# Performance work log

Hardware: AMD Instinct MI355X
Metric: run time of the kernel (lower is better)

Reference implementation:

```python
import jax, jax.numpy as jnp
import numpy as np

DIM = 768
NUM_HEADS = 8
ETA = 1e-5
LN_EPS = 1e-5
NORM_EPS = 1e-12  # torch F.normalize clamp_min


def setup_inputs() -> dict:
    key = jax.random.key(0)
    ks = jax.random.split(key, 4)
    B, N, C = 8, 4096, DIM
    x = jax.random.normal(ks[0], (B, N, C), dtype=jnp.float32)
    # torch nn.Linear weight layout: [out, in]; qkv_bias=False per init_kwargs
    qkv_w = jax.random.normal(ks[1], (3 * C, C), dtype=jnp.float32) * (C ** -0.5)
    proj_w = jax.random.normal(ks[2], (C, C), dtype=jnp.float32) * (C ** -0.5)
    proj_b = jnp.zeros((C,), dtype=jnp.float32)
    ln_g = jnp.ones((C,), dtype=jnp.float32)
    ln_b = jnp.zeros((C,), dtype=jnp.float32)
    temperature = jnp.ones((NUM_HEADS, 1, 1), dtype=jnp.float32)
    gamma1 = jnp.full((C,), ETA, dtype=jnp.float32)
    return {"x": x, "qkv_w": qkv_w, "proj_w": proj_w, "proj_b": proj_b,
            "ln_g": ln_g, "ln_b": ln_b, "temperature": temperature, "gamma1": gamma1}


def _l2norm(t):
    # torch F.normalize(dim=-1): t / max(||t||_2, eps)
    n = jnp.sqrt(jnp.sum(t * t, axis=-1, keepdims=True))
    return t / jnp.maximum(n, NORM_EPS)


def reference(x, qkv_w, proj_w, proj_b, ln_g, ln_b, temperature, gamma1):
    B, N, C = x.shape
    H = NUM_HEADS
    dh = C // H
    m = x
    # LayerNorm
    mu = jnp.mean(x, axis=-1, keepdims=True)
    var = jnp.mean(jnp.square(x - mu), axis=-1, keepdims=True)
    xn = (x - mu) * jax.lax.rsqrt(var + LN_EPS) * ln_g + ln_b
    # qkv: [B,N,3C] -> [3,B,H,dh,N] (q/k/v already transposed to channels-first)
    qkv = jnp.einsum('bnc,oc->bno', xn, qkv_w)
    qkv = qkv.reshape(B, N, 3, H, dh).transpose(2, 0, 3, 4, 1)  # [3,B,H,dh,N]
    q, k, v = qkv[0], qkv[1], qkv[2]
    q = _l2norm(q)  # normalize over tokens (last dim = N)
    k = _l2norm(k)
    # cross-covariance attention over channels: [B,H,dh,dh]
    attn = jnp.einsum('bhdn,bhen->bhde', q, k) * temperature
    attn = jax.nn.softmax(attn, axis=-1)
    # weighted channel mix: [B,H,dh,N] -> [B,N,C]
    out = jnp.einsum('bhde,bhen->bhdn', attn, v)
    out = out.transpose(0, 3, 1, 2).reshape(B, N, C)
    out = jnp.einsum('bnc,oc->bno', out, proj_w) + proj_b
    out = gamma1 * out
    return out + m
```

## Files before the change

kernel.cpp:

```cpp
#include <hip/hip_runtime.h>
#include <hip/hip_bf16.h>
#include <stdint.h>

typedef __attribute__((ext_vector_type(8))) short short8;
typedef __attribute__((ext_vector_type(4))) float f32x4;
typedef __attribute__((ext_vector_type(4))) unsigned short us4;

#define DIMC 768
#define NTOK 32768
#define NPB 4096
#define HEADS 8
#define DH 96

__device__ __forceinline__ ushort f2bf(float f) {
    union { float f; uint32_t u; } c; c.f = f;
    uint32_t u = c.u;
    u += 0x7fffu + ((u >> 16) & 1u);
    return (ushort)(u >> 16);
}
__device__ __forceinline__ float bf2f(ushort h) {
    union { uint32_t u; float f; } c; c.u = ((uint32_t)h) << 16;
    return c.f;
}

__device__ __forceinline__ void gload_lds16(const void* g, void* l) {
    __builtin_amdgcn_global_load_lds(
        (const __attribute__((address_space(1))) void*)g,
        (__attribute__((address_space(3))) void*)l, 16, 0, 0);
}

__device__ __forceinline__ void gemm256_core(
    const char* aglob, const char* bglob, char* lds, f32x4 (&acc)[8][4]) {
    const int tid = threadIdx.x;
    const int lane = tid & 63, wid = tid >> 6;
    const int wr = wid >> 2, wc = wid & 3;
    const int k8 = lane >> 4, l15 = lane & 15;

    const int L0 = tid * 16, L1 = (512 + tid) * 16;
    const int S0 = L0 ^ (((L0 >> 9) & 1) << 5);
    const int S1 = L1 ^ (((L1 >> 9) & 1) << 5);
    const int sr0 = S0 >> 6, sc0 = S0 & 63;
    const int sr1 = S1 >> 6, sc1 = S1 & 63;

    int aoff[8], boff[4];
#pragma unroll
    for (int m = 0; m < 8; m++) {
        int row = wr * 128 + m * 16 + l15;
        int o = row * 64 + k8 * 16;
        aoff[m] = o ^ (((o >> 9) & 1) << 5);
    }
#pragma unroll
    for (int n = 0; n < 4; n++) {
        int row = wc * 64 + n * 16 + l15;
        int o = row * 64 + k8 * 16;
        boff[n] = o ^ (((o >> 9) & 1) << 5);
    }

#define STG_A(kt, c) do {                                     \
        const char* ak_ = aglob + (size_t)(kt) * 64;          \
        char* al_ = lds + (c) * 16384;                        \
        gload_lds16(ak_ + sr0 * 1536 + sc0, al_ + L0);        \
        gload_lds16(ak_ + sr1 * 1536 + sc1, al_ + L1);        \
    } while (0)
#define STG_B(kt, c) do {                                     \
        const char* bk_ = bglob + (size_t)(kt) * 64;          \
        char* bl_ = lds + 32768 + (c) * 16384;                \
        gload_lds16(bk_ + sr0 * 1536 + sc0, bl_ + L0);        \
        gload_lds16(bk_ + sr1 * 1536 + sc1, bl_ + L1);        \
    } while (0)
#define MFMA16(mb)                                                                 \
    __builtin_amdgcn_s_setprio(1);                                                 \
    _Pragma("unroll")                                                              \
    for (int m_ = 0; m_ < 4; m_++)                                                 \
        _Pragma("unroll")                                                          \
        for (int n_ = 0; n_ < 4; n_++)                                             \
            acc[(mb) + m_][n_] = __builtin_amdgcn_mfma_f32_16x16x32_bf16(          \
                af[m_], bf[n_], acc[(mb) + m_][n_], 0, 0, 0);                      \
    __builtin_amdgcn_s_setprio(0);
#define BAR  asm volatile("s_barrier" ::: "memory")
#define LGKM0 do { asm volatile("s_waitcnt lgkmcnt(0)" ::: "memory"); \
                   __builtin_amdgcn_sched_barrier(0); } while (0)

    STG_B(0, 0); STG_A(0, 0); STG_B(1, 1);
    asm volatile("s_waitcnt vmcnt(2)" ::: "memory");
    BAR;

    const char* a0 = lds;
    const char* a1 = lds + 16384;
    const char* b0 = lds + 32768;
    const char* b1 = lds + 49152;

#pragma unroll
    for (int i = 0; i < 6; ++i) {
        short8 af[4], bf[4];
#pragma unroll
        for (int n = 0; n < 4; n++) bf[n] = *(const short8*)(b0 + boff[n]);
#pragma unroll
        for (int m = 0; m < 4; m++) af[m] = *(const short8*)(a0 + aoff[m]);
        STG_A(2 * i + 1, 1);
        BAR;
        LGKM0;
        MFMA16(0)
        BAR;
#pragma unroll
        for (int m = 0; m < 4; m++) af[m] = *(const short8*)(a0 + aoff[4 + m]);
        if (2 * i + 2 < 12) STG_B(2 * i + 2, 0);
        BAR;
        LGKM0;
        MFMA16(4)
        if (i < 5) asm volatile("s_waitcnt vmcnt(2)" ::: "memory");
        else       asm volatile("s_waitcnt vmcnt(0)" ::: "memory");
        BAR;
#pragma unroll
        for (int n = 0; n < 4; n++) bf[n] = *(const short8*)(b1 + boff[n]);
#pragma unroll
        for (int m = 0; m < 4; m++) af[m] = *(const short8*)(a1 + aoff[m]);
        if (2 * i + 2 < 12) STG_A(2 * i + 2, 0);
        BAR;
        LGKM0;
        MFMA16(0)
        BAR;
#pragma unroll
        for (int m = 0; m < 4; m++) af[m] = *(const short8*)(a1 + aoff[4 + m]);
        if (2 * i + 3 < 12) STG_B(2 * i + 3, 1);
        BAR;
        LGKM0;
        MFMA16(4)
        if (i < 5) {
            asm volatile("s_waitcnt vmcnt(2)" ::: "memory");
            BAR;
        }
    }
#undef STG_A
#undef STG_B
#undef MFMA16
#undef BAR
#undef LGKM0
}

__global__ __launch_bounds__(256) void prep_fused_kernel(
    const float* __restrict__ qw, const float* __restrict__ pw,
    ushort* __restrict__ qwb, ushort* __restrict__ pwb,
    const float* __restrict__ x, const float* __restrict__ g,
    const float* __restrict__ b, ushort* __restrict__ xb) {
    int bid = blockIdx.x;
    if (bid < 1728) {
        int i4 = (bid * 256 + threadIdx.x) * 4;
        if (i4 < 3 * DIMC * DIMC) {
            float4 w = *(const float4*)&qw[i4];
            us4 o;
            o[0] = f2bf(w.x); o[1] = f2bf(w.y); o[2] = f2bf(w.z); o[3] = f2bf(w.w);
            *(us4*)&qwb[i4] = o;
        }
        if (i4 < DIMC * DIMC) {
            float4 w = *(const float4*)&pw[i4];
            us4 o;
            o[0] = f2bf(w.x); o[1] = f2bf(w.y); o[2] = f2bf(w.z); o[3] = f2bf(w.w);
            *(us4*)&pwb[i4] = o;
        }
        return;
    }
    int t = (bid - 1728) * 4 + (threadIdx.x >> 6);
    int lane = threadIdx.x & 63;
    const float* xr = x + (size_t)t * DIMC;
    float4 v[3];
    float s = 0.f, s2 = 0.f;
#pragma unroll
    for (int u = 0; u < 3; u++) {
        v[u] = *(const float4*)&xr[u * 256 + lane * 4];
        s  += v[u].x + v[u].y + v[u].z + v[u].w;
        s2 += v[u].x * v[u].x + v[u].y * v[u].y + v[u].z * v[u].z + v[u].w * v[u].w;
    }
#pragma unroll
    for (int off = 32; off > 0; off >>= 1) {
        s  += __shfl_down(s, off);
        s2 += __shfl_down(s2, off);
    }
    s = __shfl(s, 0);
    s2 = __shfl(s2, 0);
    float mean = s * (1.0f / DIMC);
    float rstd = rsqrtf(s2 * (1.0f / DIMC) - mean * mean + 1e-5f);
    ushort* xo = xb + (size_t)t * DIMC;
#pragma unroll
    for (int u = 0; u < 3; u++) {
        float4 gv = *(const float4*)&g[u * 256 + lane * 4];
        float4 bv = *(const float4*)&b[u * 256 + lane * 4];
        us4 o;
        o[0] = f2bf((v[u].x - mean) * rstd * gv.x + bv.x);
        o[1] = f2bf((v[u].y - mean) * rstd * gv.y + bv.y);
        o[2] = f2bf((v[u].z - mean) * rstd * gv.z + bv.z);
        o[3] = f2bf((v[u].w - mean) * rstd * gv.w + bv.w);
        *(us4*)&xo[u * 256 + lane * 4] = o;
    }
}

__global__ __launch_bounds__(512) void gemm_qkv_kernel(
    const ushort* __restrict__ xb, const ushort* __restrict__ wb,
    ushort* __restrict__ qb, ushort* __restrict__ kb, ushort* __restrict__ vb) {
    __shared__ __align__(16) char lds[65536];
    int orig = blockIdx.x;
    int wg = (orig & 7) * 144 + (orig >> 3);
    int nt = wg % 9, mt = wg / 9;
    int m0 = mt * 256, n0 = nt * 256;
    f32x4 acc[8][4] = {};
    gemm256_core((const char*)(xb + (size_t)m0 * DIMC),
                 (const char*)(wb + (size_t)n0 * DIMC), lds, acc);

    int tid = threadIdx.x, lane = tid & 63, wid = tid >> 6;
    int wr = wid >> 2, wc = wid & 3;
    int k8 = lane >> 4, l15 = lane & 15;
    int seg = n0 / DIMC;
#pragma unroll
    for (int m8 = 0; m8 < 8; m8++) {
        int r0 = m0 + wr * 128 + m8 * 16 + k8 * 4;
        int b_ = r0 >> 12, nn = r0 & (NPB - 1);
#pragma unroll
        for (int n = 0; n < 4; n++) {
            int o = n0 + wc * 64 + n * 16 + l15;
            f32x4 a = acc[m8][n];
            if (seg == 2) {
                int oL = o - 2 * DIMC;
#pragma unroll
                for (int qq = 0; qq < 4; qq++)
                    vb[(size_t)(r0 + qq) * DIMC + oL] = f2bf(a[qq]);
            } else {
                int oL = o - seg * DIMC;
                int h = oL / DH, d = oL - h * DH;
                us4 pk;
#pragma unroll
                for (int qq = 0; qq < 4; qq++) pk[qq] = f2bf(a[qq]);
                *(us4*)((seg ? kb : qb) +
                        ((size_t)(b_ * HEADS + h) * DH + d) * NPB + nn) = pk;
            }
        }
    }
}

__global__ __launch_bounds__(576) void attn_qk_kernel(
    const ushort* __restrict__ qb, const ushort* __restrict__ kb,
    float* __restrict__ S, float* __restrict__ S2) {
    int bh = blockIdx.x, ch = blockIdx.y;
    int tid = threadIdx.x, wid = tid >> 6, lane = tid & 63;
    int wr = wid / 3, wc = wid - wr * 3;
    int k8 = lane >> 4, l15 = lane & 15;
    const ushort* qrow = qb + (size_t)bh * DH * NPB + ch * 512;
    const ushort* krow = kb + (size_t)bh * DH * NPB + ch * 512;
    bool doq = (wc == 0), dok = (wr == 0);
    f32x4 acc[2][2] = {};
    float sq[2] = {0.f, 0.f}, sk[2] = {0.f, 0.f};
    for (int n = 0; n < 512; n += 32) {
        short8 a[2], b[2];
#pragma unroll
        for (int i = 0; i < 2; i++)
            a[i] = *(const short8*)&qrow[(size_t)(wr * 32 + i * 16 + l15) * NPB + n + k8 * 8];
#pragma unroll
        for (int j = 0; j < 2; j++)
            b[j] = *(const short8*)&krow[(size_t)(wc * 32 + j * 16 + l15) * NPB + n + k8 * 8];
        if (doq) {
#pragma unroll
            for (int i = 0; i < 2; i++)
#pragma unroll
                for (int u = 0; u < 8; u++) {
                    float f = bf2f((ushort)a[i][u]); sq[i] += f * f;
                }
        }
        if (dok) {
#pragma unroll
            for (int j = 0; j < 2; j++)
#pragma unroll
                for (int u = 0; u < 8; u++) {
                    float f = bf2f((ushort)b[j][u]); sk[j] += f * f;
                }
        }
#pragma unroll
        for (int i = 0; i < 2; i++)
#pragma unroll
            for (int j = 0; j < 2; j++)
                acc[i][j] = __builtin_amdgcn_mfma_f32_16x16x32_bf16(a[i], b[j], acc[i][j], 0, 0, 0);
    }
    float* S2o = S2 + ((size_t)ch * 64 + bh) * 192;
    if (doq) {
#pragma unroll
        for (int i = 0; i < 2; i++) {
            float v = sq[i];
            v += __shfl_xor(v, 16); v += __shfl_xor(v, 32);
            if (lane < 16) S2o[wr * 32 + i * 16 + l15] = v;
        }
    }
    if (dok) {
#pragma unroll
        for (int j = 0; j < 2; j++) {
            float v = sk[j];
            v += __shfl_xor(v, 16); v += __shfl_xor(v, 32);
            if (lane < 16) S2o[96 + wc * 32 + j * 16 + l15] = v;
        }
    }
    float* So = S + ((size_t)ch * 64 + bh) * (DH * DH);
#pragma unroll
    for (int i = 0; i < 2; i++)
#pragma unroll
        for (int j = 0; j < 2; j++) {
            int e = wc * 32 + j * 16 + l15;
#pragma unroll
            for (int qq = 0; qq < 4; qq++) {
                int d = wr * 32 + i * 16 + k8 * 4 + qq;
                So[d * DH + e] = acc[i][j][qq];
            }
        }
}

__global__ __launch_bounds__(192) void attn_soft_kernel(
    const float* __restrict__ S, const float* __restrict__ S2,
    const float* __restrict__ temp, ushort* __restrict__ attnT) {
    int bh = blockIdx.x, ds0 = blockIdx.y * 32;
    int tid = threadIdx.x, r = tid & 31, p = tid >> 5;
    int d = ds0 + r;
    __shared__ float rkv[96];
    if (tid < 96) {
        float sum = 0.f;
#pragma unroll 1
        for (int ch = 0; ch < 8; ch++)
            sum += S2[((size_t)ch * 64 + bh) * 192 + 96 + tid];
        rkv[tid] = 1.0f / fmaxf(sqrtf(sum), 1e-12f);
    }
    float sqd = 0.f;
#pragma unroll 1
    for (int ch = 0; ch < 8; ch++)
        sqd += S2[((size_t)ch * 64 + bh) * 192 + d];
    float rqd = 1.0f / fmaxf(sqrtf(sqd), 1e-12f);
    float4 v[4] = {};
#pragma unroll 1
    for (int ch = 0; ch < 8; ch++) {
        const float* So = S + (((size_t)ch * 64 + bh) * DH + d) * DH + p * 16;
#pragma unroll
        for (int u = 0; u < 4; u++) {
            float4 w = *(const float4*)&So[u * 4];
            v[u].x += w.x; v[u].y += w.y; v[u].z += w.z; v[u].w += w.w;
        }
    }
    __syncthreads();
    float sd = rqd * temp[bh & (HEADS - 1)];
#pragma unroll
    for (int u = 0; u < 4; u++) {
        int e0 = p * 16 + u * 4;
        v[u].x *= sd * rkv[e0]; v[u].y *= sd * rkv[e0 + 1];
        v[u].z *= sd * rkv[e0 + 2]; v[u].w *= sd * rkv[e0 + 3];
    }
    __shared__ float red[32][8], red2[32][8];
    float lm = -3.4e38f;
#pragma unroll
    for (int u = 0; u < 4; u++)
        lm = fmaxf(lm, fmaxf(fmaxf(v[u].x, v[u].y), fmaxf(v[u].z, v[u].w)));
    red[r][p] = lm;
    __syncthreads();
    float m = red[r][0];
#pragma unroll
    for (int u = 1; u < 6; u++) m = fmaxf(m, red[r][u]);
    float s = 0.f;
#pragma unroll
    for (int u = 0; u < 4; u++) {
        v[u].x = __expf(v[u].x - m); v[u].y = __expf(v[u].y - m);
        v[u].z = __expf(v[u].z - m); v[u].w = __expf(v[u].w - m);
        s += v[u].x + v[u].y + v[u].z + v[u].w;
    }
    red2[r][p] = s;
    __syncthreads();
    float tot = red2[r][0];
#pragma unroll
    for (int u = 1; u < 6; u++) tot += red2[r][u];
    float inv = 1.0f / tot;
    ushort* ao = attnT + (size_t)bh * (DH * DH) + d;
#pragma unroll
    for (int u = 0; u < 4; u++) {
        int e0 = p * 16 + u * 4;
        ao[(e0 + 0) * DH] = f2bf(v[u].x * inv);
        ao[(e0 + 1) * DH] = f2bf(v[u].y * inv);
        ao[(e0 + 2) * DH] = f2bf(v[u].z * inv);
        ao[(e0 + 3) * DH] = f2bf(v[u].w * inv);
    }
}

__global__ __launch_bounds__(256) void w2prep_kernel(
    const ushort* __restrict__ pwb, const ushort* __restrict__ attnT,
    ushort* __restrict__ W2) {
    int bh = blockIdx.x, o0 = blockIdx.y * 256;
    int b_ = bh >> 3, h = bh & 7;
    int tid = threadIdx.x, wid = tid >> 6, lane = tid & 63;
    int k8 = lane >> 4, l15 = lane & 15;
    const ushort* at = attnT + (size_t)bh * (DH * DH);
    f32x4 acc[4][6] = {};
#pragma unroll
    for (int kk = 0; kk < DH; kk += 32) {
        short8 af[4], bf[6];
#pragma unroll
        for (int m = 0; m < 4; m++)
            af[m] = *(const short8*)&pwb[(size_t)(o0 + wid * 64 + m * 16 + l15) * DIMC
                                         + h * DH + kk + k8 * 8];
#pragma unroll
        for (int n = 0; n < 6; n++)
            bf[n] = *(const short8*)&at[(n * 16 + l15) * DH + kk + k8 * 8];
#pragma unroll
        for (int m = 0; m < 4; m++)
#pragma unroll
            for (int n = 0; n < 6; n++)
                acc[m][n] = __builtin_amdgcn_mfma_f32_16x16x32_bf16(af[m], bf[n], acc[m][n], 0, 0, 0);
    }
    ushort* wo = W2 + (size_t)b_ * DIMC * DIMC + (size_t)h * DH;
#pragma unroll
    for (int m = 0; m < 4; m++) {
        int orow = o0 + wid * 64 + m * 16 + k8 * 4;
#pragma unroll
        for (int n = 0; n < 6; n++) {
            int e = n * 16 + l15;
#pragma unroll
            for (int qq = 0; qq < 4; qq++)
                wo[(size_t)(orow + qq) * DIMC + e] = f2bf(acc[m][n][qq]);
        }
    }
}

__global__ __launch_bounds__(512) void vproj_kernel(
    const ushort* __restrict__ vb, const ushort* __restrict__ W2,
    const float* __restrict__ pb, const float* __restrict__ g1,
    const float* __restrict__ x, float* __restrict__ out) {
    __shared__ __align__(16) char lds[65536];
    int orig = blockIdx.x;
    int wg = (orig & 7) * 48 + (orig >> 3);
    int b_ = wg / 48, rem = wg % 48, mt = rem / 3, ntl = rem % 3;
    int tok0 = b_ * NPB + mt * 256, o0 = ntl * 256;
    f32x4 acc[8][4] = {};
    gemm256_core((const char*)(vb + (size_t)tok0 * DIMC),
                 (const char*)(W2 + (size_t)b_ * DIMC * DIMC + (size_t)o0 * DIMC),
                 lds, acc);

    int tid = threadIdx.x, lane = tid & 63, wid = tid >> 6;
    int wr = wid >> 2, wc = wid & 3;
    int k8 = lane >> 4, l15 = lane & 15;
#pragma unroll
    for (int m8 = 0; m8 < 8; m8++) {
        int r0 = tok0 + wr * 128 + m8 * 16 + k8 * 4;
#pragma unroll
        for (int n = 0; n < 4; n++) {
            int o = o0 + wc * 64 + n * 16 + l15;
            float pbo = pb[o], g1o = g1[o];
            f32x4 a = acc[m8][n];
#pragma unroll
            for (int qq = 0; qq < 4; qq++) {
                size_t idx = (size_t)(r0 + qq) * DIMC + o;
                out[idx] = g1o * (a[qq] + pbo) + x[idx];
            }
        }
    }
}

extern "C" void kernel_launch(void* const* d_in, const int* in_sizes, int n_in,
                              void* d_out, int out_size, void* d_ws, size_t ws_size,
                              hipStream_t stream) {
    const float* x     = (const float*)d_in[0];
    const float* qkvw  = (const float*)d_in[1];
    const float* projw = (const float*)d_in[2];
    const float* projb = (const float*)d_in[3];
    const float* lng   = (const float*)d_in[4];
    const float* lnb   = (const float*)d_in[5];
    const float* temp  = (const float*)d_in[6];
    const float* g1    = (const float*)d_in[7];
    float* out = (float*)d_out;

    char* w = (char*)d_ws;
    ushort* qb    = (ushort*)(w + 0);
    ushort* kb    = (ushort*)(w + 50331648);
    ushort* vb    = (ushort*)(w + 100663296);
    ushort* qwb   = (ushort*)(w + 150994944);
    ushort* pwb   = (ushort*)(w + 154533888);
    float*  S2    = (float*)(w + 155713536);
    ushort* attnT = qwb;
    ushort* W2    = qb;
    ushort* xb    = (ushort*)d_out;
    float*  S     = (float*)((char*)d_out + 50331648);

    hipLaunchKernelGGL(prep_fused_kernel, dim3(9920), dim3(256), 0, stream,
                       qkvw, projw, qwb, pwb, x, lng, lnb, xb);
    hipLaunchKernelGGL(gemm_qkv_kernel, dim3(1152), dim3(512), 0, stream,
                       xb, qwb, qb, kb, vb);
    hipLaunchKernelGGL(attn_qk_kernel, dim3(64, 8), dim3(576), 0, stream,
                       qb, kb, S, S2);
    hipLaunchKernelGGL(attn_soft_kernel, dim3(64, 3), dim3(192), 0, stream,
                       S, S2, temp, attnT);
    hipLaunchKernelGGL(w2prep_kernel, dim3(64, 3), dim3(256), 0, stream,
                       pwb, attnT, W2);
    hipLaunchKernelGGL(vproj_kernel, dim3(384), dim3(512), 0, stream,
                       vb, W2, projb, g1, x, out);
}
```

Baseline: 253.5 us.

## Fuse softmax and W2 prep into one kernel, store partial scores as bf16

The separate softmax and W2-prep kernels are merged into one attn_finish kernel with one block per batch-head. The softmaxed attention now stays in LDS and feeds the MFMA projection directly, which drops a launch and a global round trip. The partial QK score tiles are also written as bf16 instead of fp32, halving that traffic. In exchange the fused stage runs only 64 blocks instead of 192 per stage, so parallelism is lower, and summing bf16 partials across chunks costs some precision.

```diff
diff --git a/kernel.cpp b/kernel.cpp
--- a/kernel.cpp
+++ b/kernel.cpp
@@ -238,7 +238,7 @@
 
 __global__ __launch_bounds__(576) void attn_qk_kernel(
     const ushort* __restrict__ qb, const ushort* __restrict__ kb,
-    float* __restrict__ S, float* __restrict__ S2) {
+    ushort* __restrict__ S, float* __restrict__ S2) {
     int bh = blockIdx.x, ch = blockIdx.y;
     int tid = threadIdx.x, wid = tid >> 6, lane = tid & 63;
     int wr = wid / 3, wc = wid - wr * 3;
@@ -295,7 +295,7 @@
             if (lane < 16) S2o[96 + wc * 32 + j * 16 + l15] = v;
         }
     }
-    float* So = S + ((size_t)ch * 64 + bh) * (DH * DH);
+    ushort* So = S + ((size_t)ch * 64 + bh) * (DH * DH);
 #pragma unroll
     for (int i = 0; i < 2; i++)
 #pragma unroll
@@ -304,18 +304,22 @@
 #pragma unroll
             for (int qq = 0; qq < 4; qq++) {
                 int d = wr * 32 + i * 16 + k8 * 4 + qq;
-                So[d * DH + e] = acc[i][j][qq];
+                So[d * DH + e] = f2bf(acc[i][j][qq]);
             }
         }
 }
 
-__global__ __launch_bounds__(192) void attn_soft_kernel(
-    const float* __restrict__ S, const float* __restrict__ S2,
-    const float* __restrict__ temp, ushort* __restrict__ attnT) {
-    int bh = blockIdx.x, ds0 = blockIdx.y * 32;
-    int tid = threadIdx.x, r = tid & 31, p = tid >> 5;
-    int d = ds0 + r;
+__global__ __launch_bounds__(576) void attn_finish_kernel(
+    const ushort* __restrict__ S, const float* __restrict__ S2,
+    const float* __restrict__ temp, const ushort* __restrict__ pwb,
+    ushort* __restrict__ W2) {
+    int bh = blockIdx.x;
+    int b_ = bh >> 3, h = bh & 7;
+    int tid = threadIdx.x;
     __shared__ float rkv[96];
+    __shared__ float red[96][6], red2[96][6];
+    __shared__ ushort atl[96][104];
+    int r = tid % 96, p = tid / 96;
     if (tid < 96) {
         float sum = 0.f;
 #pragma unroll 1
@@ -326,31 +330,29 @@
     float sqd = 0.f;
 #pragma unroll 1
     for (int ch = 0; ch < 8; ch++)
-        sqd += S2[((size_t)ch * 64 + bh) * 192 + d];
+        sqd += S2[((size_t)ch * 64 + bh) * 192 + r];
     float rqd = 1.0f / fmaxf(sqrtf(sqd), 1e-12f);
-    float4 v[4] = {};
+    float v[16];
+#pragma unroll
+    for (int u = 0; u < 16; u++) v[u] = 0.f;
 #pragma unroll 1
     for (int ch = 0; ch < 8; ch++) {
-        const float* So = S + (((size_t)ch * 64 + bh) * DH + d) * DH + p * 16;
-#pragma unroll
-        for (int u = 0; u < 4; u++) {
-            float4 w = *(const float4*)&So[u * 4];
-            v[u].x += w.x; v[u].y += w.y; v[u].z += w.z; v[u].w += w.w;
+        const ushort* So = S + ((size_t)ch * 64 + bh) * (DH * DH) + r * DH + p * 16;
+        short8 w0 = *(const short8*)So;
+        short8 w1 = *(const short8*)(So + 8);
+#pragma unroll
+        for (int u = 0; u < 8; u++) {
+            v[u] += bf2f((ushort)w0[u]);
+            v[8 + u] += bf2f((ushort)w1[u]);
         }
     }
     __syncthreads();
-    float sd = rqd * temp[bh & (HEADS - 1)];
-#pragma unroll
-    for (int u = 0; u < 4; u++) {
-        int e0 = p * 16 + u * 4;
-        v[u].x *= sd * rkv[e0]; v[u].y *= sd * rkv[e0 + 1];
-        v[u].z *= sd * rkv[e0 + 2]; v[u].w *= sd * rkv[e0 + 3];
-    }
-    __shared__ float red[32][8], red2[32][8];
-    float lm = -3.4e38f;
-#pragma unroll
-    for (int u = 0; u < 4; u++)
-        lm = fmaxf(lm, fmaxf(fmaxf(v[u].x, v[u].y), fmaxf(v[u].z, v[u].w)));
+    float sd = rqd * temp[h];
+#pragma unroll
+    for (int u = 0; u < 16; u++) v[u] *= sd * rkv[p * 16 + u];
+    float lm = v[0];
+#pragma unroll
+    for (int u = 1; u < 16; u++) lm = fmaxf(lm, v[u]);
     red[r][p] = lm;
     __syncthreads();
     float m = red[r][0];
@@ -358,63 +360,53 @@
     for (int u = 1; u < 6; u++) m = fmaxf(m, red[r][u]);
     float s = 0.f;
 #pragma unroll
-    for (int u = 0; u < 4; u++) {
-        v[u].x = __expf(v[u].x - m); v[u].y = __expf(v[u].y - m);
-        v[u].z = __expf(v[u].z - m); v[u].w = __expf(v[u].w - m);
-        s += v[u].x + v[u].y + v[u].z + v[u].w;
-    }
+    for (int u = 0; u < 16; u++) { v[u] = __expf(v[u] - m); s += v[u]; }
     red2[r][p] = s;
     __syncthreads();
     float tot = red2[r][0];
 #pragma unroll
     for (int u = 1; u < 6; u++) tot += red2[r][u];
     float inv = 1.0f / tot;
-    ushort* ao = attnT + (size_t)bh * (DH * DH) + d;
-#pragma unroll
-    for (int u = 0; u < 4; u++) {
-        int e0 = p * 16 + u * 4;
-        ao[(e0 + 0) * DH] = f2bf(v[u].x * inv);
-        ao[(e0 + 1) * DH] = f2bf(v[u].y * inv);
-        ao[(e0 + 2) * DH] = f2bf(v[u].z * inv);
-        ao[(e0 + 3) * DH] = f2bf(v[u].w * inv);
-    }
-}
-
-__global__ __launch_bounds__(256) void w2prep_kernel(
-    const ushort* __restrict__ pwb, const ushort* __restrict__ attnT,
-    ushort* __restrict__ W2) {
-    int bh = blockIdx.x, o0 = blockIdx.y * 256;
-    int b_ = bh >> 3, h = bh & 7;
-    int tid = threadIdx.x, wid = tid >> 6, lane = tid & 63;
-    int k8 = lane >> 4, l15 = lane & 15;
-    const ushort* at = attnT + (size_t)bh * (DH * DH);
-    f32x4 acc[4][6] = {};
-#pragma unroll
-    for (int kk = 0; kk < DH; kk += 32) {
-        short8 af[4], bf[6];
-#pragma unroll
-        for (int m = 0; m < 4; m++)
-            af[m] = *(const short8*)&pwb[(size_t)(o0 + wid * 64 + m * 16 + l15) * DIMC
-                                         + h * DH + kk + k8 * 8];
-#pragma unroll
-        for (int n = 0; n < 6; n++)
-            bf[n] = *(const short8*)&at[(n * 16 + l15) * DH + kk + k8 * 8];
-#pragma unroll
-        for (int m = 0; m < 4; m++)
-#pragma unroll
-            for (int n = 0; n < 6; n++)
-                acc[m][n] = __builtin_amdgcn_mfma_f32_16x16x32_bf16(af[m], bf[n], acc[m][n], 0, 0, 0);
-    }
-    ushort* wo = W2 + (size_t)b_ * DIMC * DIMC + (size_t)h * DH;
-#pragma unroll
-    for (int m = 0; m < 4; m++) {
-        int orow = o0 + wid * 64 + m * 16 + k8 * 4;
-#pragma unroll
-        for (int n = 0; n < 6; n++) {
-            int e = n * 16 + l15;
-#pragma unroll
-            for (int qq = 0; qq < 4; qq++)
-                wo[(size_t)(orow + qq) * DIMC + e] = f2bf(acc[m][n][qq]);
+#pragma unroll
+    for (int u = 0; u < 16; u++)
+        atl[p * 16 + u][r] = f2bf(v[u] * inv);
+    __syncthreads();
+    int wid = tid >> 6, lane = tid & 63;
+    if (wid < 8) {
+        int k8 = lane >> 4, l15 = lane & 15;
+        ushort* wo = W2 + (size_t)b_ * DIMC * DIMC + (size_t)h * DH;
+#pragma unroll
+        for (int pass = 0; pass < 2; pass++) {
+            int o0 = wid * 96 + pass * 48;
+            f32x4 acc[3][6] = {};
+#pragma unroll
+            for (int kk = 0; kk < DH; kk += 32) {
+                short8 af[3], bf[6];
+#pragma unroll
+                for (int mm = 0; mm < 3; mm++)
+                    af[mm] = *(const short8*)&pwb[(size_t)(o0 + mm * 16 + l15) * DIMC
+                                                  + h * DH + kk + k8 * 8];
+#pragma unroll
+                for (int n = 0; n < 6; n++)
+                    bf[n] = *(const short8*)&atl[n * 16 + l15][kk + k8 * 8];
+#pragma unroll
+                for (int mm = 0; mm < 3; mm++)
+#pragma unroll
+                    for (int n = 0; n < 6; n++)
+                        acc[mm][n] = __builtin_amdgcn_mfma_f32_16x16x32_bf16(
+                            af[mm], bf[n], acc[mm][n], 0, 0, 0);
+            }
+#pragma unroll
+            for (int mm = 0; mm < 3; mm++) {
+                int orow = o0 + mm * 16 + k8 * 4;
+#pragma unroll
+                for (int n = 0; n < 6; n++) {
+                    int e = n * 16 + l15;
+#pragma unroll
+                    for (int qq = 0; qq < 4; qq++)
+                        wo[(size_t)(orow + qq) * DIMC + e] = f2bf(acc[mm][n][qq]);
+                }
+            }
         }
     }
 }
@@ -473,21 +465,18 @@
     ushort* qwb   = (ushort*)(w + 150994944);
     ushort* pwb   = (ushort*)(w + 154533888);
     float*  S2    = (float*)(w + 155713536);
-    ushort* attnT = qwb;
     ushort* W2    = qb;
     ushort* xb    = (ushort*)d_out;
-    float*  S     = (float*)((char*)d_out + 50331648);
+    ushort* Sb    = (ushort*)((char*)d_out + 50331648);
 
     hipLaunchKernelGGL(prep_fused_kernel, dim3(9920), dim3(256), 0, stream,
                        qkvw, projw, qwb, pwb, x, lng, lnb, xb);
     hipLaunchKernelGGL(gemm_qkv_kernel, dim3(1152), dim3(512), 0, stream,
                        xb, qwb, qb, kb, vb);
     hipLaunchKernelGGL(attn_qk_kernel, dim3(64, 8), dim3(576), 0, stream,
-                       qb, kb, S, S2);
-    hipLaunchKernelGGL(attn_soft_kernel, dim3(64, 3), dim3(192), 0, stream,
-                       S, S2, temp, attnT);
-    hipLaunchKernelGGL(w2prep_kernel, dim3(64, 3), dim3(256), 0, stream,
-                       pwb, attnT, W2);
+                       qb, kb, Sb, S2);
+    hipLaunchKernelGGL(attn_finish_kernel, dim3(64), dim3(576), 0, stream,
+                       Sb, S2, temp, pwb, W2);
     hipLaunchKernelGGL(vproj_kernel, dim3(384), dim3(512), 0, stream,
                        vb, W2, projb, g1, x, out);
 }
```

Measured after the change: 253.5 us. No clear change (-0.0%).
